# Performance work log

Measured on AMD Instinct MI355X. Metric: run time of the kernel, lower is better.

## Reference

```python
import jax, jax.numpy as jnp
import numpy as np

NB, NL, V, VOCAB, D, TOPK = 16, 64, 16384, 32000, 256, 16
NITER, EARLY, RW = 8, 2, 0.8


def setup_inputs():
    key = jax.random.key(0)
    ks = jax.random.split(key, 8)
    probas = jax.random.uniform(ks[0], (NB, NL, V), dtype=jnp.float32) + 1e-6
    h_d = jax.random.normal(ks[1], (NB, NL, D), dtype=jnp.float32)
    lengths = jax.random.randint(ks[2], (NB,), NL // 2, NL + 1)
    mask = (jnp.arange(NL)[None, :] < lengths[:, None]).astype(jnp.int32)  # prefix mask
    batch_vocab = jax.random.randint(ks[3], (V,), 0, VOCAB)
    emb_table = jax.random.normal(ks[4], (VOCAB, D), dtype=jnp.float32) * 0.02
    W1 = jax.random.normal(ks[5], (2 * D, D), dtype=jnp.float32) * 0.006
    b1 = jnp.zeros((D,), dtype=jnp.float32)
    return {"probas": probas, "h_d": h_d, "mask": mask, "batch_vocab": batch_vocab,
            "emb_table": emb_table, "W1": W1, "b1": b1}


def _forward(probas, h_d, mask, batch_vocab, emb_table, W1, b1):
    maskf = mask.astype(probas.dtype)
    MAP = jnp.argmax(probas, axis=-1)                       # [nb,nl]
    topk_vals, topk_idx = jax.lax.top_k(probas, TOPK)       # [nb,nl,K]
    topk_vals = jnp.where(mask[..., None] < 1, 1.0, topk_vals)
    logits = jnp.log(topk_vals)                             # Categorical(probs) == categorical(log p)
    sLens = jnp.sum(mask, axis=1)                           # [nb]
    one_hot = jnp.arange(NL)[None, :] == (sLens - 1)[:, None]  # one_hot_by_mask: last valid pos
    m2d = (mask[:, :, None] * mask[:, None, :]) > 0
    eyeM = jnp.eye(NL, dtype=probas.dtype)
    h_masked = h_d * maskf[..., None]

    def step(carry, k):
        max_score, best, count, stopped = carry
        choice = jax.random.categorical(k, logits)          # [nb,nl]
        samples = jnp.take_along_axis(topk_idx, choice[..., None], axis=-1)[..., 0]
        samples = jnp.where(one_hot, MAP, samples)
        embs = emb_table[batch_vocab[samples]] * maskf[..., None]   # gather+embed, masked
        new_embs = jax.nn.relu(jnp.concatenate([embs, h_masked], axis=-1) @ W1 + b1)
        Kmat = jnp.einsum('bld,bmd->blm', new_embs, new_embs)       # [nb,nl,nl]
        # det of leading lxl submatrix == det with padded rows/cols replaced by identity
        score = jnp.linalg.det(jnp.where(m2d, Kmat, eyeM))          # [nb]
        improved = score > max_score
        any_imp = jnp.any(improved)
        count = jnp.where(any_imp, 0, count + 1)
        upd = improved & (~stopped)
        stopped = stopped | ((~any_imp) & (count >= EARLY))
        max_score = jnp.where(upd, score, max_score)
        best = jnp.where(upd[:, None], samples, best)
        return (max_score, best, count, stopped), None

    init = (jnp.full((NB,), -jnp.inf, probas.dtype), MAP, jnp.int32(0), jnp.bool_(False))
    keys = jax.random.split(jax.random.key(42), NITER)
    (max_score, best, _, _), _ = jax.lax.scan(step, init, keys)

    # diverse_proba: scatter redist_weight at best choice, (1-rw) elsewhere, renormalize
    am = jnp.where(jnp.arange(V)[None, None, :] == best[:, :, None], RW, 1.0 - RW).astype(probas.dtype)
    x = probas * am
    nm = jnp.sum(x, axis=-1, keepdims=True)
    nm = jnp.where(maskf[..., None] == 0, 1e-10, nm)
    return x / nm, max_score


def reference(probas, h_d, mask, batch_vocab, emb_table, W1, b1):
    return _forward(probas, h_d, mask, batch_vocab, emb_table, W1, b1)
```

## Files before the change

### kernel.cpp

```cpp
#include <hip/hip_runtime.h>
#include <math.h>
#include <stdint.h>


#define TINYF 1.17549435082228750797e-38f

#define KMX(r, c) (((r) * 68) + ((c) ^ ((((r) >> 3) & 7) << 2)))

struct Keys16 { uint32_t k[16]; };

__host__ __device__ inline void tf2x32(uint32_t k0, uint32_t k1,
                                       uint32_t x0, uint32_t x1,
                                       uint32_t* o0, uint32_t* o1) {
  uint32_t ks2 = k0 ^ k1 ^ 0x1BD11BDAu;
  uint32_t ks[3] = {k0, k1, ks2};
  uint32_t v0 = x0 + k0, v1 = x1 + k1;
  const int R0[4] = {13, 15, 26, 6};
  const int R1[4] = {17, 29, 16, 24};
#pragma unroll
  for (int g = 0; g < 5; ++g) {
    const int* RR = (g & 1) ? R1 : R0;
#pragma unroll
    for (int r = 0; r < 4; ++r) {
      v0 += v1;
      v1 = (v1 << RR[r]) | (v1 >> (32 - RR[r]));
      v1 ^= v0;
    }
    v0 += ks[(g + 1) % 3];
    v1 += ks[(g + 2) % 3] + (uint32_t)(g + 1);
  }
  *o0 = v0; *o1 = v1;
}

__device__ inline float logf_ref(float x) { return (float)log((double)x); }

__device__ inline unsigned long long u64max(unsigned long long a,
                                            unsigned long long b) {
  return (a > b) ? a : b;
}

__device__ inline float lane_bcast_f32(float v, int slane) {
  return __uint_as_float(
      (unsigned)__builtin_amdgcn_readlane(__float_as_int(v), slane));
}

__global__ __launch_bounds__(256) void k_topk(const float* __restrict__ probas,
                                              const int* __restrict__ mask,
                                              int* __restrict__ topk_idx,
                                              float* __restrict__ logits,
                                              float* __restrict__ S) {
  int row = blockIdx.x;
  int t = threadIdx.x;
  const float* p = probas + (size_t)row * 16384;
  __shared__ unsigned long long lists[256][16];
  __shared__ float swsum[4];
  __shared__ int lcnt;
  unsigned long long* cand = &lists[0][0];

  cand[t] = 0ull;
  cand[t + 256] = 0ull;
  if (t == 0) lcnt = 0;
  __syncthreads();

  const uint32_t TB = 0x3F7E0000u;
  float sum = 0.f;
  const float4* p4 = (const float4*)p;
#pragma unroll 4
  for (int j = 0; j < 16; ++j) {
    float4 x = p4[t + j * 256];
    int v0 = (t + j * 256) * 4;
    uint32_t u0 = __float_as_uint(x.x), u1 = __float_as_uint(x.y);
    uint32_t u2 = __float_as_uint(x.z), u3 = __float_as_uint(x.w);
    sum += x.x; sum += x.y; sum += x.z; sum += x.w;
    uint32_t um = max(max(u0, u1), max(u2, u3));
    if (um >= TB) {
      if (u0 >= TB) { int s = atomicAdd(&lcnt, 1); if (s < 512)
          cand[s] = ((unsigned long long)u0 << 32) | (unsigned)(~(v0 + 0)); }
      if (u1 >= TB) { int s = atomicAdd(&lcnt, 1); if (s < 512)
          cand[s] = ((unsigned long long)u1 << 32) | (unsigned)(~(v0 + 1)); }
      if (u2 >= TB) { int s = atomicAdd(&lcnt, 1); if (s < 512)
          cand[s] = ((unsigned long long)u2 << 32) | (unsigned)(~(v0 + 2)); }
      if (u3 >= TB) { int s = atomicAdd(&lcnt, 1); if (s < 512)
          cand[s] = ((unsigned long long)u3 << 32) | (unsigned)(~(v0 + 3)); }
    }
  }
#pragma unroll
  for (int off = 32; off >= 1; off >>= 1) sum += __shfl_down(sum, off);
  if ((t & 63) == 0) swsum[t >> 6] = sum;
  __syncthreads();
  if (t == 0) S[row] = ((swsum[0] + swsum[1]) + swsum[2]) + swsum[3];

  int n = lcnt;
  if (n >= 16 && n <= 512) {
    if (t < 64) {
      unsigned long long c[8];
#pragma unroll
      for (int k = 0; k < 8; ++k) c[k] = cand[t + 64 * k];
      unsigned long long win = 0ull;
#pragma unroll
      for (int r = 0; r < 16; ++r) {
        unsigned long long m = c[0];
#pragma unroll
        for (int k = 1; k < 8; ++k) m = u64max(m, c[k]);
#pragma unroll
        for (int off = 32; off >= 1; off >>= 1) {
          unsigned long long o = __shfl_xor(m, off);
          m = u64max(m, o);
        }
        if (t == r) win = m;
#pragma unroll
        for (int k = 0; k < 8; ++k) if (c[k] == m) c[k] = 0ull;
      }
      if (t < 16) {
        int idx = (int)(~(unsigned)(win & 0xFFFFFFFFull));
        float val = __uint_as_float((unsigned)(win >> 32));
        topk_idx[row * 16 + t] = idx;
        logits[row * 16 + t] = (mask[row] == 0) ? 0.0f : logf_ref(val);
      }
    }
    return;
  }

  {
    unsigned long long loc[16];
#pragma unroll
    for (int q = 0; q < 16; ++q) loc[q] = 0ull;
    for (int j = 0; j < 64; ++j) {
      int v = t + j * 256;
      float x = p[v];
      unsigned long long key =
          ((unsigned long long)__float_as_uint(x) << 32) | (unsigned)(~v);
      if (key > loc[15]) {
        loc[15] = key;
#pragma unroll
        for (int q = 15; q > 0; --q) {
          if (loc[q] > loc[q - 1]) {
            unsigned long long tmp = loc[q]; loc[q] = loc[q - 1]; loc[q - 1] = tmp;
          }
        }
      }
    }
    __syncthreads();
#pragma unroll
    for (int q = 0; q < 16; ++q) lists[t][q] = loc[q];
    __syncthreads();
    for (int nl = 128; nl >= 1; nl >>= 1) {
      if (t < nl) {
        unsigned long long M[16];
        int ia = 0, ib = 0;
#pragma unroll
        for (int q = 0; q < 16; ++q) {
          unsigned long long av = lists[t][ia];
          unsigned long long bv = lists[t + nl][ib];
          if (av >= bv) { M[q] = av; ia++; } else { M[q] = bv; ib++; }
        }
#pragma unroll
        for (int q = 0; q < 16; ++q) lists[t][q] = M[q];
      }
      __syncthreads();
    }
    if (t < 16) {
      unsigned long long key = lists[0][t];
      int idx = (int)(~(unsigned)(key & 0xFFFFFFFFull));
      float val = __uint_as_float((unsigned)(key >> 32));
      topk_idx[row * 16 + t] = idx;
      logits[row * 16 + t] = (mask[row] == 0) ? 0.0f : logf_ref(val);
    }
  }
}

__global__ __launch_bounds__(256) void k_sample(Keys16 keys,
                                                const int* __restrict__ mask,
                                                const int* __restrict__ topk_idx,
                                                const float* __restrict__ logits,
                                                int* __restrict__ samples,
                                                int* __restrict__ choice) {
  int tid = blockIdx.x * 256 + threadIdx.x;
  int i = tid >> 10;
  int rbl = tid & 1023;
  int b = rbl >> 6;
  int l = rbl & 63;
  uint32_t k0 = keys.k[2 * i], k1 = keys.k[2 * i + 1];
  int sl = 0;
  for (int m = 0; m < 64; ++m) sl += mask[b * 64 + m];
  float bestv = 0.f; int bestk = 0;
#pragma unroll
  for (int k = 0; k < 16; ++k) {
    uint32_t j = (uint32_t)((b * 64 + l) * 16 + k);
    uint32_t y0, y1;
    tf2x32(k0, k1, 0u, j, &y0, &y1);
    uint32_t bits = y0 ^ y1;
    float f = __uint_as_float((bits >> 9) | 0x3f800000u) - 1.0f;
    float u = fmaxf(TINYF, f * 1.0f + TINYF);
    float t1 = logf_ref(u);
    float g = -logf_ref(-t1);
    float sv = g + logits[rbl * 16 + k];
    if (k == 0 || sv > bestv) { bestv = sv; bestk = k; }
  }
  int ce = (l == sl - 1) ? 0 : bestk;
  choice[tid] = ce;
  samples[tid] = topk_idx[rbl * 16 + ce];
}

__global__ __launch_bounds__(256) void k_ce(const int* __restrict__ topk_idx,
                                            const int* __restrict__ batch_vocab,
                                            const float* __restrict__ emb,
                                            const float* __restrict__ W1,
                                            const float* __restrict__ h_d,
                                            const float* __restrict__ b1,
                                            const int* __restrict__ mask,
                                            float* __restrict__ Eall) {
  int row = blockIdx.x;
  int t = threadIdx.x;
  __shared__ int rid[16];
  __shared__ float e[16][256];
  __shared__ float hl[256];
  float mkf = (float)mask[row];
  if (t < 16) rid[t] = batch_vocab[topk_idx[row * 16 + t]];
  hl[t] = h_d[(size_t)row * 256 + t] * mkf;
  __syncthreads();
#pragma unroll
  for (int k = 0; k < 16; ++k) e[k][t] = emb[(size_t)rid[k] * 256 + t];
  __syncthreads();
  float acch = 0.f;
  for (int j0 = 0; j0 < 256; j0 += 4) {
    float4 hv = *(const float4*)&hl[j0];
    float w0 = W1[(256 + j0 + 0) * 256 + t];
    float w1 = W1[(256 + j0 + 1) * 256 + t];
    float w2 = W1[(256 + j0 + 2) * 256 + t];
    float w3 = W1[(256 + j0 + 3) * 256 + t];
    acch = fmaf(hv.x, w0, acch);
    acch = fmaf(hv.y, w1, acch);
    acch = fmaf(hv.z, w2, acch);
    acch = fmaf(hv.w, w3, acch);
  }
  float acc[16];
#pragma unroll
  for (int k = 0; k < 16; ++k) acc[k] = 0.f;
  for (int j0 = 0; j0 < 256; j0 += 4) {
    float w0 = W1[(j0 + 0) * 256 + t];
    float w1 = W1[(j0 + 1) * 256 + t];
    float w2 = W1[(j0 + 2) * 256 + t];
    float w3 = W1[(j0 + 3) * 256 + t];
#pragma unroll
    for (int k = 0; k < 16; ++k) {
      float4 ev = *(const float4*)&e[k][j0];
      acc[k] = fmaf(ev.x, w0, acc[k]);
      acc[k] = fmaf(ev.y, w1, acc[k]);
      acc[k] = fmaf(ev.z, w2, acc[k]);
      acc[k] = fmaf(ev.w, w3, acc[k]);
    }
  }
  float b1v = b1[t];
#pragma unroll
  for (int k = 0; k < 16; ++k) {
    float val = fmaf(mkf, acc[k], acch) + b1v;
    Eall[((size_t)row * 16 + k) * 256 + t] = fmaxf(val, 0.0f);
  }
}

__global__ __launch_bounds__(256, 1) void k_gram(const float* __restrict__ Eall,
                                                 const int* __restrict__ mask,
                                                 const int* __restrict__ choice,
                                                 float* __restrict__ scores) {
  int blk = blockIdx.x;
  int i = blk >> 4, b = blk & 15;
  int t = threadIdx.x;
  __shared__ __align__(16) float Ett[64][68];
  __shared__ __align__(16) float KmF[64 * 68];
  __shared__ int ch[64];
  int mskv = 0;
  if (t < 64) {
    ch[t] = choice[i * 1024 + b * 64 + t];
    mskv = mask[b * 64 + t];
  }
  __syncthreads();
  int l = t & 63, wd = t >> 6;
  const float* eptr =
      Eall + ((size_t)((b * 64 + l) * 16 + ch[l])) * 256 + wd * 16;
  float acc[16];
#pragma unroll
  for (int q = 0; q < 16; ++q) acc[q] = 0.f;
  int tx = t & 15, ty = t >> 4;
  for (int dt = 0; dt < 4; ++dt) {
    const float* src = eptr + dt * 64;
    float4 v0 = *(const float4*)(src + 0);
    float4 v1 = *(const float4*)(src + 4);
    float4 v2 = *(const float4*)(src + 8);
    float4 v3 = *(const float4*)(src + 12);
    int d0 = wd * 16;
    Ett[d0 +  0][l] = v0.x; Ett[d0 +  1][l] = v0.y;
    Ett[d0 +  2][l] = v0.z; Ett[d0 +  3][l] = v0.w;
    Ett[d0 +  4][l] = v1.x; Ett[d0 +  5][l] = v1.y;
    Ett[d0 +  6][l] = v1.z; Ett[d0 +  7][l] = v1.w;
    Ett[d0 +  8][l] = v2.x; Ett[d0 +  9][l] = v2.y;
    Ett[d0 + 10][l] = v2.z; Ett[d0 + 11][l] = v2.w;
    Ett[d0 + 12][l] = v3.x; Ett[d0 + 13][l] = v3.y;
    Ett[d0 + 14][l] = v3.z; Ett[d0 + 15][l] = v3.w;
    __syncthreads();
#pragma unroll 4
    for (int dd = 0; dd < 64; ++dd) {
      float4 av4 = *(const float4*)&Ett[dd][tx * 4];
      float4 bv4 = *(const float4*)&Ett[dd][ty * 4];
      float avv[4] = {av4.x, av4.y, av4.z, av4.w};
      float bvv[4] = {bv4.x, bv4.y, bv4.z, bv4.w};
#pragma unroll
      for (int a2 = 0; a2 < 4; ++a2)
#pragma unroll
        for (int c2 = 0; c2 < 4; ++c2)
          acc[a2 * 4 + c2] = fmaf(avv[a2], bvv[c2], acc[a2 * 4 + c2]);
    }
    __syncthreads();
  }
#pragma unroll
  for (int a2 = 0; a2 < 4; ++a2)
#pragma unroll
    for (int c2 = 0; c2 < 4; ++c2)
      KmF[KMX(tx * 4 + a2, ty * 4 + c2)] = acc[a2 * 4 + c2];
  __syncthreads();
  if (t >= 64) return;

  unsigned long long bal = __ballot(mskv != 0);
  int L = __popcll(bal);

  float km[64];
#pragma unroll
  for (int c0 = 0; c0 < 64; c0 += 4) {
    float4 v = *(const float4*)&KmF[KMX(t, c0)];
    km[c0 + 0] = v.x; km[c0 + 1] = v.y; km[c0 + 2] = v.z; km[c0 + 3] = v.w;
  }

  float sdet = 1.f, ssign = 1.f;
  int pos = t;

#pragma unroll
  for (int p = 0; p < 64; ++p) {
    if (p < L) {
      bool cnd = (pos >= p) && (pos < L);
      unsigned lo = (((unsigned)(63 - pos)) << 6) | (unsigned)t;
      unsigned long long key =
          cnd ? ((((unsigned long long)__float_as_uint(fabsf(km[p]))) << 32) | lo)
              : 0ull;
#pragma unroll
      for (int off = 32; off >= 1; off >>= 1) {
        unsigned long long o = __shfl_xor(key, off);
        if (o > key) key = o;
      }
      int lane_rb = (int)(key & 63u);
      int pb = 63 - (int)((key >> 6) & 63u);
      int srb = __builtin_amdgcn_readfirstlane(lane_rb);
      float kpp = lane_bcast_f32(km[p], srb);
      sdet *= kpp;
      if (pb != p) ssign = -ssign;
      int np = pos;
      if (pos == p) np = pb;
      if (t == lane_rb) np = p;
      pos = np;
      bool active = (pos > p) && (pos < L);
      float f = (active && kpp != 0.f) ? (km[p] / kpp) : 0.f;
      float nf = -f;
#pragma unroll
      for (int c = p + 1; c < 64; ++c) {
        float pr = lane_bcast_f32(km[c], srb);
        if (active) km[c] = fmaf(nf, pr, km[c]);
      }
    }
  }
  if (t == 0) scores[i * 16 + b] = sdet * ssign;
}

__global__ __launch_bounds__(256) void k_out(const float* __restrict__ probas,
                                             const int* __restrict__ mask,
                                             const int* __restrict__ samples,
                                             const int* __restrict__ topk_idx,
                                             const float* __restrict__ scores,
                                             const float* __restrict__ S,
                                             float* __restrict__ out,
                                             float* __restrict__ out_ms) {
  int row = blockIdx.x;
  int b = row >> 6;
  int t = threadIdx.x;
  __shared__ float ssc[128];
  if (t < 128) ssc[t] = scores[t];
  __syncthreads();
  float ms[16]; int w[16];
#pragma unroll
  for (int q = 0; q < 16; ++q) { ms[q] = -INFINITY; w[q] = -1; }
  int count = 0; bool stopped = false;
#pragma unroll
  for (int i = 0; i < 8; ++i) {
    bool any = false; bool imp[16];
#pragma unroll
    for (int q = 0; q < 16; ++q) {
      imp[q] = ssc[i * 16 + q] > ms[q];
      any = any || imp[q];
    }
    count = any ? 0 : (count + 1);
#pragma unroll
    for (int q = 0; q < 16; ++q) {
      if (imp[q] && !stopped) { ms[q] = ssc[i * 16 + q]; w[q] = i; }
    }
    stopped = stopped || ((!any) && (count >= 2));
  }
  if (row == 0 && t == 0) {
#pragma unroll
    for (int q = 0; q < 16; ++q) out_ms[q] = ms[q];
  }
  int wi = -1;
#pragma unroll
  for (int q = 0; q < 16; ++q) if (b == q) wi = w[q];

  int best = (wi >= 0) ? samples[wi * 1024 + row] : topk_idx[row * 16];
  const float* p = probas + (size_t)row * 16384;
  float* o = out + (size_t)row * 16384;
  float nm;
  if (mask[row] == 0) {
    nm = 1e-10f;
  } else {
    nm = 0.2f * S[row] + 0.6f * p[best];
  }
  const float4* p4 = (const float4*)p;
  float4* o4 = (float4*)o;
  for (int f = t; f < 4096; f += 256) {
    float4 x = p4[f];
    int v0 = f << 2;
    float4 r;
    r.x = x.x * ((v0 + 0 == best) ? 0.8f : 0.2f) / nm;
    r.y = x.y * ((v0 + 1 == best) ? 0.8f : 0.2f) / nm;
    r.z = x.z * ((v0 + 2 == best) ? 0.8f : 0.2f) / nm;
    r.w = x.w * ((v0 + 3 == best) ? 0.8f : 0.2f) / nm;
    o4[f] = r;
  }
}

extern "C" void kernel_launch(void* const* d_in, const int* in_sizes, int n_in,
                              void* d_out, int out_size, void* d_ws, size_t ws_size,
                              hipStream_t stream) {
  const float* probas = (const float*)d_in[0];
  const float* h_d    = (const float*)d_in[1];
  const int*   mask   = (const int*)d_in[2];
  const int*   bvoc   = (const int*)d_in[3];
  const float* emb    = (const float*)d_in[4];
  const float* W1     = (const float*)d_in[5];
  const float* b1     = (const float*)d_in[6];
  float* out = (float*)d_out;

  char* w = (char*)d_ws;
  int*   topk_idx = (int*)w;   w += 16384 * sizeof(int);
  float* logits   = (float*)w; w += 16384 * sizeof(float);
  float* S        = (float*)w; w += 1024 * sizeof(float);
  int*   samples  = (int*)w;   w += 8192 * sizeof(int);
  int*   choice   = (int*)w;   w += 8192 * sizeof(int);
  float* scores   = (float*)w; w += 128 * sizeof(float);

  float* Eall = out;

  Keys16 keys;
  for (uint32_t i = 0; i < 8; ++i) {
    uint32_t a, bq;
    tf2x32(0u, 42u, 0u, i, &a, &bq);
    keys.k[2 * i] = a; keys.k[2 * i + 1] = bq;
  }

  k_topk<<<1024, 256, 0, stream>>>(probas, mask, topk_idx, logits, S);
  k_sample<<<32, 256, 0, stream>>>(keys, mask, topk_idx, logits, samples, choice);
  k_ce<<<1024, 256, 0, stream>>>(topk_idx, bvoc, emb, W1, h_d, b1, mask, Eall);
  k_gram<<<128, 256, 0, stream>>>(Eall, mask, choice, scores);
  k_out<<<1024, 256, 0, stream>>>(probas, mask, samples, topk_idx, scores, S,
                                  out, out + 16777216);
}
```

Before: 306.4 us.

## Process two rows per block in embedding MLP and loop LU elimination dynamically

The candidate-embedding kernel now handles two rows per block, so each W1 column load is reused across 32 candidate embeddings. Embedding and h_d vectors are read directly from global memory through wave-uniform row indices instead of being staged in shared memory, and the grid is halved. The determinant kernel's elimination loop becomes a runtime loop up to L. It carries the pivot column in a register and updates 8-column chunks, with whole chunks skipped once they fall left of the pivot. This cuts code size and skips padded iterations, at the cost of more registers in the MLP kernel and more redundant work on partially active chunks.

New measurement: 487.5 us. 1.59x slower.

```diff
diff --git a/kernel.cpp b/kernel.cpp
--- a/kernel.cpp
+++ b/kernel.cpp
@@ -210,52 +210,68 @@
                                             const float* __restrict__ b1,
                                             const int* __restrict__ mask,
                                             float* __restrict__ Eall) {
-  int row = blockIdx.x;
+  int row0 = blockIdx.x * 2;
   int t = threadIdx.x;
-  __shared__ int rid[16];
-  __shared__ float e[16][256];
-  __shared__ float hl[256];
-  float mkf = (float)mask[row];
-  if (t < 16) rid[t] = batch_vocab[topk_idx[row * 16 + t]];
-  hl[t] = h_d[(size_t)row * 256 + t] * mkf;
-  __syncthreads();
-#pragma unroll
-  for (int k = 0; k < 16; ++k) e[k][t] = emb[(size_t)rid[k] * 256 + t];
-  __syncthreads();
-  float acch = 0.f;
+  int rid[2][16];
+  int mk01[2];
+#pragma unroll
+  for (int r = 0; r < 2; ++r) {
+    mk01[r] = __builtin_amdgcn_readfirstlane(mask[row0 + r]);
+#pragma unroll
+    for (int k = 0; k < 16; ++k) {
+      int ti = topk_idx[(row0 + r) * 16 + k];
+      rid[r][k] = __builtin_amdgcn_readfirstlane(batch_vocab[ti]);
+    }
+  }
+  float acch[2] = {0.f, 0.f};
   for (int j0 = 0; j0 < 256; j0 += 4) {
-    float4 hv = *(const float4*)&hl[j0];
     float w0 = W1[(256 + j0 + 0) * 256 + t];
     float w1 = W1[(256 + j0 + 1) * 256 + t];
     float w2 = W1[(256 + j0 + 2) * 256 + t];
     float w3 = W1[(256 + j0 + 3) * 256 + t];
-    acch = fmaf(hv.x, w0, acch);
-    acch = fmaf(hv.y, w1, acch);
-    acch = fmaf(hv.z, w2, acch);
-    acch = fmaf(hv.w, w3, acch);
-  }
-  float acc[16];
-#pragma unroll
-  for (int k = 0; k < 16; ++k) acc[k] = 0.f;
+#pragma unroll
+    for (int r = 0; r < 2; ++r) {
+      float4 hv = *(const float4*)&h_d[(size_t)(row0 + r) * 256 + j0];
+      acch[r] = fmaf(hv.x, w0, acch[r]);
+      acch[r] = fmaf(hv.y, w1, acch[r]);
+      acch[r] = fmaf(hv.z, w2, acch[r]);
+      acch[r] = fmaf(hv.w, w3, acch[r]);
+    }
+  }
+#pragma unroll
+  for (int r = 0; r < 2; ++r)
+    if (mk01[r] == 0) acch[r] = 0.0f;
+  float acc[2][16];
+#pragma unroll
+  for (int r = 0; r < 2; ++r)
+#pragma unroll
+    for (int k = 0; k < 16; ++k) acc[r][k] = 0.f;
   for (int j0 = 0; j0 < 256; j0 += 4) {
     float w0 = W1[(j0 + 0) * 256 + t];
     float w1 = W1[(j0 + 1) * 256 + t];
     float w2 = W1[(j0 + 2) * 256 + t];
     float w3 = W1[(j0 + 3) * 256 + t];
 #pragma unroll
+    for (int r = 0; r < 2; ++r) {
+#pragma unroll
+      for (int k = 0; k < 16; ++k) {
+        float4 ev = *(const float4*)&emb[(size_t)rid[r][k] * 256 + j0];
+        acc[r][k] = fmaf(ev.x, w0, acc[r][k]);
+        acc[r][k] = fmaf(ev.y, w1, acc[r][k]);
+        acc[r][k] = fmaf(ev.z, w2, acc[r][k]);
+        acc[r][k] = fmaf(ev.w, w3, acc[r][k]);
+      }
+    }
+  }
+  float b1v = b1[t];
+#pragma unroll
+  for (int r = 0; r < 2; ++r) {
+    float mkf = (float)mk01[r];
+#pragma unroll
     for (int k = 0; k < 16; ++k) {
-      float4 ev = *(const float4*)&e[k][j0];
-      acc[k] = fmaf(ev.x, w0, acc[k]);
-      acc[k] = fmaf(ev.y, w1, acc[k]);
-      acc[k] = fmaf(ev.z, w2, acc[k]);
-      acc[k] = fmaf(ev.w, w3, acc[k]);
-    }
-  }
-  float b1v = b1[t];
-#pragma unroll
-  for (int k = 0; k < 16; ++k) {
-    float val = fmaf(mkf, acc[k], acch) + b1v;
-    Eall[((size_t)row * 16 + k) * 256 + t] = fmaxf(val, 0.0f);
+      float val = fmaf(mkf, acc[r][k], acch[r]) + b1v;
+      Eall[((size_t)(row0 + r) * 16 + k) * 256 + t] = fmaxf(val, 0.0f);
+    }
   }
 }
 
@@ -332,39 +348,49 @@
 
   float sdet = 1.f, ssign = 1.f;
   int pos = t;
-
-#pragma unroll
-  for (int p = 0; p < 64; ++p) {
-    if (p < L) {
-      bool cnd = (pos >= p) && (pos < L);
-      unsigned lo = (((unsigned)(63 - pos)) << 6) | (unsigned)t;
-      unsigned long long key =
-          cnd ? ((((unsigned long long)__float_as_uint(fabsf(km[p]))) << 32) | lo)
-              : 0ull;
-#pragma unroll
-      for (int off = 32; off >= 1; off >>= 1) {
-        unsigned long long o = __shfl_xor(key, off);
-        if (o > key) key = o;
-      }
-      int lane_rb = (int)(key & 63u);
-      int pb = 63 - (int)((key >> 6) & 63u);
-      int srb = __builtin_amdgcn_readfirstlane(lane_rb);
-      float kpp = lane_bcast_f32(km[p], srb);
-      sdet *= kpp;
-      if (pb != p) ssign = -ssign;
-      int np = pos;
-      if (pos == p) np = pb;
-      if (t == lane_rb) np = p;
-      pos = np;
-      bool active = (pos > p) && (pos < L);
-      float f = (active && kpp != 0.f) ? (km[p] / kpp) : 0.f;
-      float nf = -f;
-#pragma unroll
-      for (int c = p + 1; c < 64; ++c) {
-        float pr = lane_bcast_f32(km[c], srb);
-        if (active) km[c] = fmaf(nf, pr, km[c]);
-      }
-    }
+  float curcol = km[0];
+
+#pragma unroll 1
+  for (int p = 0; p < L; ++p) {
+    bool cnd = (pos >= p) && (pos < L);
+    unsigned lo = (((unsigned)(63 - pos)) << 6) | (unsigned)t;
+    unsigned long long key =
+        cnd ? ((((unsigned long long)__float_as_uint(fabsf(curcol))) << 32) | lo)
+            : 0ull;
+#pragma unroll
+    for (int off = 32; off >= 1; off >>= 1) {
+      unsigned long long o = __shfl_xor(key, off);
+      if (o > key) key = o;
+    }
+    int lane_rb = (int)(key & 63u);
+    int pb = 63 - (int)((key >> 6) & 63u);
+    int srb = __builtin_amdgcn_readfirstlane(lane_rb);
+    float kpp = lane_bcast_f32(curcol, srb);
+    sdet *= kpp;
+    if (pb != p) ssign = -ssign;
+    int np = pos;
+    if (pos == p) np = pb;
+    if (t == lane_rb) np = p;
+    pos = np;
+    bool active = (pos > p) && (pos < L);
+    float f = (active && kpp != 0.f) ? (curcol / kpp) : 0.f;
+    float nf = -f;
+    float ncc = curcol;
+    int pp1 = p + 1;
+#pragma unroll
+    for (int chk = 0; chk < 8; ++chk) {
+      if (chk * 8 + 7 >= pp1) {
+#pragma unroll
+        for (int cc = 0; cc < 8; ++cc) {
+          const int c = chk * 8 + cc;
+          float pr = lane_bcast_f32(km[c], srb);
+          float nv = fmaf(nf, pr, km[c]);
+          km[c] = nv;
+          ncc = (c == pp1) ? nv : ncc;
+        }
+      }
+    }
+    curcol = ncc;
   }
   if (t == 0) scores[i * 16 + b] = sdet * ssign;
 }
@@ -464,7 +490,7 @@
 
   k_topk<<<1024, 256, 0, stream>>>(probas, mask, topk_idx, logits, S);
   k_sample<<<32, 256, 0, stream>>>(keys, mask, topk_idx, logits, samples, choice);
-  k_ce<<<1024, 256, 0, stream>>>(topk_idx, bvoc, emb, W1, h_d, b1, mask, Eall);
+  k_ce<<<512, 256, 0, stream>>>(topk_idx, bvoc, emb, W1, h_d, b1, mask, Eall);
   k_gram<<<128, 256, 0, stream>>>(Eall, mask, choice, scores);
   k_out<<<1024, 256, 0, stream>>>(probas, mask, samples, topk_idx, scores, S,
                                   out, out + 16777216);
```

## Compute embeddings only for top-k candidates actually sampled across iterations

Applied to the files above, without the earlier changes.

k_ce now gathers which of the 16 top-k candidates were chosen by any of the 8 sampling iterations for each row. It runs the embedding MLP only for those, up to 8 compact slots instead of all 16, and k_gram maps each choice to its compacted slot index via popcount. The determinant elimination loop is also changed from a fully unrolled 64-step loop to a runtime loop bounded by L, with chunked column updates and a carried current pivot column. This cuts the k_ce FLOPs and Eall traffic roughly in half, but adds atomics and an extra sync, and drops the per-column active predicate in the update.

Measured after the change: 297.9 us. 1.03x faster.

```diff
diff --git a/kernel.cpp b/kernel.cpp
--- a/kernel.cpp
+++ b/kernel.cpp
@@ -209,18 +209,36 @@
                                             const float* __restrict__ h_d,
                                             const float* __restrict__ b1,
                                             const int* __restrict__ mask,
+                                            const int* __restrict__ choice,
                                             float* __restrict__ Eall) {
   int row = blockIdx.x;
   int t = threadIdx.x;
-  __shared__ int rid[16];
-  __shared__ float e[16][256];
+  __shared__ int smb;
+  __shared__ int rid[8];
+  __shared__ float e[8][256];
   __shared__ float hl[256];
+  if (t == 0) smb = 0;
   float mkf = (float)mask[row];
-  if (t < 16) rid[t] = batch_vocab[topk_idx[row * 16 + t]];
   hl[t] = h_d[(size_t)row * 256 + t] * mkf;
   __syncthreads();
-#pragma unroll
-  for (int k = 0; k < 16; ++k) e[k][t] = emb[(size_t)rid[k] * 256 + t];
+  if (t < 8) atomicOr(&smb, 1 << choice[t * 1024 + row]);
+  __syncthreads();
+  int mb = smb;
+  if (t < 8) {
+    int cnt = __popc(mb);
+    int ss = (t < cnt) ? t : 0;
+    int kk = 0;
+    for (int bit = 0; bit < 16; ++bit) {
+      if ((mb >> bit) & 1) {
+        if (ss == 0) { kk = bit; break; }
+        ss--;
+      }
+    }
+    rid[t] = batch_vocab[topk_idx[row * 16 + kk]];
+  }
+  __syncthreads();
+#pragma unroll
+  for (int k = 0; k < 8; ++k) e[k][t] = emb[(size_t)rid[k] * 256 + t];
   __syncthreads();
   float acch = 0.f;
   for (int j0 = 0; j0 < 256; j0 += 4) {
@@ -234,16 +252,16 @@
     acch = fmaf(hv.z, w2, acch);
     acch = fmaf(hv.w, w3, acch);
   }
-  float acc[16];
-#pragma unroll
-  for (int k = 0; k < 16; ++k) acc[k] = 0.f;
+  float acc[8];
+#pragma unroll
+  for (int k = 0; k < 8; ++k) acc[k] = 0.f;
   for (int j0 = 0; j0 < 256; j0 += 4) {
     float w0 = W1[(j0 + 0) * 256 + t];
     float w1 = W1[(j0 + 1) * 256 + t];
     float w2 = W1[(j0 + 2) * 256 + t];
     float w3 = W1[(j0 + 3) * 256 + t];
 #pragma unroll
-    for (int k = 0; k < 16; ++k) {
+    for (int k = 0; k < 8; ++k) {
       float4 ev = *(const float4*)&e[k][j0];
       acc[k] = fmaf(ev.x, w0, acc[k]);
       acc[k] = fmaf(ev.y, w1, acc[k]);
@@ -253,9 +271,9 @@
   }
   float b1v = b1[t];
 #pragma unroll
-  for (int k = 0; k < 16; ++k) {
+  for (int k = 0; k < 8; ++k) {
     float val = fmaf(mkf, acc[k], acch) + b1v;
-    Eall[((size_t)row * 16 + k) * 256 + t] = fmaxf(val, 0.0f);
+    Eall[((size_t)row * 8 + k) * 256 + t] = fmaxf(val, 0.0f);
   }
 }
 
@@ -271,13 +289,18 @@
   __shared__ int ch[64];
   int mskv = 0;
   if (t < 64) {
-    ch[t] = choice[i * 1024 + b * 64 + t];
-    mskv = mask[b * 64 + t];
+    int rowi = b * 64 + t;
+    int ml = 0;
+#pragma unroll
+    for (int ii = 0; ii < 8; ++ii) ml |= 1 << choice[ii * 1024 + rowi];
+    int cc = choice[i * 1024 + rowi];
+    ch[t] = __popc(ml & ((1 << cc) - 1));
+    mskv = mask[rowi];
   }
   __syncthreads();
   int l = t & 63, wd = t >> 6;
   const float* eptr =
-      Eall + ((size_t)((b * 64 + l) * 16 + ch[l])) * 256 + wd * 16;
+      Eall + ((size_t)((b * 64 + l) * 8 + ch[l])) * 256 + wd * 16;
   float acc[16];
 #pragma unroll
   for (int q = 0; q < 16; ++q) acc[q] = 0.f;
@@ -332,39 +355,49 @@
 
   float sdet = 1.f, ssign = 1.f;
   int pos = t;
-
-#pragma unroll
-  for (int p = 0; p < 64; ++p) {
-    if (p < L) {
-      bool cnd = (pos >= p) && (pos < L);
-      unsigned lo = (((unsigned)(63 - pos)) << 6) | (unsigned)t;
-      unsigned long long key =
-          cnd ? ((((unsigned long long)__float_as_uint(fabsf(km[p]))) << 32) | lo)
-              : 0ull;
-#pragma unroll
-      for (int off = 32; off >= 1; off >>= 1) {
-        unsigned long long o = __shfl_xor(key, off);
-        if (o > key) key = o;
+  float curcol = km[0];
+
+#pragma unroll 1
+  for (int p = 0; p < L; ++p) {
+    bool cnd = (pos >= p) && (pos < L);
+    unsigned lo = (((unsigned)(63 - pos)) << 6) | (unsigned)t;
+    unsigned long long key =
+        cnd ? ((((unsigned long long)__float_as_uint(fabsf(curcol))) << 32) | lo)
+            : 0ull;
+#pragma unroll
+    for (int off = 32; off >= 1; off >>= 1) {
+      unsigned long long o = __shfl_xor(key, off);
+      if (o > key) key = o;
+    }
+    int lane_rb = (int)(key & 63u);
+    int pb = 63 - (int)((key >> 6) & 63u);
+    int srb = __builtin_amdgcn_readfirstlane(lane_rb);
+    float kpp = lane_bcast_f32(curcol, srb);
+    sdet *= kpp;
+    if (pb != p) ssign = -ssign;
+    int np = pos;
+    if (pos == p) np = pb;
+    if (t == lane_rb) np = p;
+    pos = np;
+    bool active = (pos > p) && (pos < L);
+    float f = (active && kpp != 0.f) ? (curcol / kpp) : 0.f;
+    float nf = -f;
+    float ncc = curcol;
+    int pp1 = p + 1;
+#pragma unroll
+    for (int chk = 0; chk < 8; ++chk) {
+      if (chk * 8 + 7 >= pp1) {
+#pragma unroll
+        for (int cc = 0; cc < 8; ++cc) {
+          const int c = chk * 8 + cc;
+          float pr = lane_bcast_f32(km[c], srb);
+          float nv = fmaf(nf, pr, km[c]);
+          km[c] = nv;
+          ncc = (c == pp1) ? nv : ncc;
+        }
       }
-      int lane_rb = (int)(key & 63u);
-      int pb = 63 - (int)((key >> 6) & 63u);
-      int srb = __builtin_amdgcn_readfirstlane(lane_rb);
-      float kpp = lane_bcast_f32(km[p], srb);
-      sdet *= kpp;
-      if (pb != p) ssign = -ssign;
-      int np = pos;
-      if (pos == p) np = pb;
-      if (t == lane_rb) np = p;
-      pos = np;
-      bool active = (pos > p) && (pos < L);
-      float f = (active && kpp != 0.f) ? (km[p] / kpp) : 0.f;
-      float nf = -f;
-#pragma unroll
-      for (int c = p + 1; c < 64; ++c) {
-        float pr = lane_bcast_f32(km[c], srb);
-        if (active) km[c] = fmaf(nf, pr, km[c]);
-      }
-    }
+    }
+    curcol = ncc;
   }
   if (t == 0) scores[i * 16 + b] = sdet * ssign;
 }
@@ -464,7 +497,8 @@
 
   k_topk<<<1024, 256, 0, stream>>>(probas, mask, topk_idx, logits, S);
   k_sample<<<32, 256, 0, stream>>>(keys, mask, topk_idx, logits, samples, choice);
-  k_ce<<<1024, 256, 0, stream>>>(topk_idx, bvoc, emb, W1, h_d, b1, mask, Eall);
+  k_ce<<<1024, 256, 0, stream>>>(topk_idx, bvoc, emb, W1, h_d, b1, mask, choice,
+                                 Eall);
   k_gram<<<128, 256, 0, stream>>>(Eall, mask, choice, scores);
   k_out<<<1024, 256, 0, stream>>>(probas, mask, samples, topk_idx, scores, S,
                                   out, out + 16777216);
```
